# Optimization experiments

Hardware: AMD Instinct MI355X
Metric: run time of the kernel (lower is better)

## Reference

```python
import jax, jax.numpy as jnp
import numpy as np

N, K = 256, 133
INPUT_W, INPUT_H = 256, 256
SPLIT = 2.0
W = round(INPUT_W * SPLIT)  # 512
H = round(INPUT_H * SPLIT)  # 512
SIGMA = (5.66, 5.66)
BETA = 10.0
LABEL_BETA = 10.0


def setup_inputs() -> dict:
    key = jax.random.key(0)
    k1, k2, k3 = jax.random.split(key, 3)
    pred = jax.random.normal(k1, (N, K, W + H), dtype=jnp.float32)
    xy = jax.random.uniform(k2, (N, K, 2), dtype=jnp.float32) * INPUT_W
    vis = (jax.random.uniform(k3, (N, K, 1), dtype=jnp.float32) > 0.2).astype(jnp.float32)
    keypoints = jnp.concatenate([xy, vis], axis=-1)
    return {"pred": pred, "keypoints": keypoints}


def _gaussian_targets(keypoints):
    # Vectorized equivalent of the Python (n,k) loop in gaussian_smoothng.
    kp_xy = keypoints[..., :2]
    vis = keypoints[..., 2]
    mu = jnp.round(kp_xy * SPLIT)  # int64 in torch; rounded float is numerically identical
    rx = SIGMA[0] * 3.0
    ry = SIGMA[1] * 3.0
    left = mu[..., 0] - rx
    right = mu[..., 0] + rx + 1.0
    top = mu[..., 1] - ry
    bottom = mu[..., 1] + ry + 1.0
    oob = (left >= W) | (top >= H) | (right < 0) | (bottom < 0)
    visible = vis >= 0.5
    valid = visible & (~oob)
    x = jnp.arange(W, dtype=jnp.float32)
    y = jnp.arange(H, dtype=jnp.float32)
    gx = jnp.exp(-((x[None, None, :] - mu[..., 0:1]) ** 2) / (2.0 * SIGMA[0] ** 2))
    gy = jnp.exp(-((y[None, None, :] - mu[..., 1:2]) ** 2) / (2.0 * SIGMA[1] ** 2))
    target_x = jnp.where(valid[..., None], gx, 0.0)  # (N,K,W)
    target_y = jnp.where(valid[..., None], gy, 0.0)  # (N,K,H)
    # weight = visible value, zeroed if visible but out of bounds
    weight = jnp.where(visible & oob, 0.0, vis)
    return target_x, target_y, weight


def _criterion(p, t):
    # p, t: (N*K, L). KLDivLoss(reduction='none') then mean over dim=1.
    log_pt = jax.nn.log_softmax(p * BETA, axis=1)
    lab = jax.nn.softmax(t * LABEL_BETA, axis=1)  # strictly positive
    kl = lab * (jnp.log(lab) - log_pt)
    return kl.mean(axis=1)


def reference(pred, keypoints):
    n, k, _ = pred.shape
    split = pred.shape[-1] // 2
    pred_x = pred[..., :split].reshape(-1, split)
    pred_y = pred[..., split:].reshape(-1, pred.shape[-1] - split)
    gt_x, gt_y, w = _gaussian_targets(keypoints)
    w = w.reshape(-1)
    loss_x = (_criterion(pred_x, gt_x.reshape(-1, W)) * w).sum()
    loss_y = (_criterion(pred_y, gt_y.reshape(-1, H)) * w).sum()
    return (loss_x + loss_y) / k
```

## Files before the change

### kernel.cpp

```cpp
#include <hip/hip_runtime.h>
#include <math.h>

#define NKP 133
#define NROWS (256 * NKP)
#define RH_TOTAL (2 * NROWS)
#define NQUADS (RH_TOTAL / 4)
#define NBLOCKS 2048
#define NWAVES (NBLOCKS * 4)
#define C2P  14.4269504088896f
#define NK2  0.02251706f
#define RAD  16.98f
#define LN2f 0.69314718055994531f

static __device__ __forceinline__ float fexp2(float x) { return __builtin_amdgcn_exp2f(x); }
static __device__ __forceinline__ float frcp (float x) { return __builtin_amdgcn_rcpf(x); }

__global__ __launch_bounds__(256) void rtmcc_partial_kernel(
    const float* __restrict__ pred,
    const float* __restrict__ keypoints,
    float* __restrict__ partials)
{
    const int wave = threadIdx.x >> 6;
    const int lane = threadIdx.x & 63;
    const int g    = lane >> 4;
    const int l4   = lane & 15;
    const int h    = g & 1;
    __shared__ float t_em1[256];
    __shared__ float t_eg [256];
    __shared__ float lds[4];

    {
        const int t = threadIdx.x;
        const float d = (float)(t - 128);
        float em1 = 0.0f, eg = 0.0f;
        if (fabsf(d) <= 35.0f) {
            const float gg = fexp2(-d * d * NK2);
            const float e  = fexp2(gg * C2P);
            em1 = e - 1.0f; eg = e * gg;
        }
        t_em1[t] = em1; t_eg[t] = eg;
    }
    __syncthreads();

    float acc = 0.0f;
    const int wid = blockIdx.x * 4 + wave;

    int q = wid;
    {
        const int row = 2 * q + (g >> 1);
        float kx = keypoints[row * 3 + 0];
        float ky = keypoints[row * 3 + 1];
        float kv = keypoints[row * 3 + 2];

        for (; q < NQUADS; q += NWAVES) {
            const float kxc = kx, kyc = ky, kvc = kv;
            const int qn = q + NWAVES;
            if (qn < NQUADS) {
                const int rown = 2 * qn + (g >> 1);
                kx = keypoints[rown * 3 + 0];
                ky = keypoints[rown * 3 + 1];
                kv = keypoints[rown * 3 + 2];
            }

            const float mux = rintf(kxc * 2.0f);
            const float muy = rintf(kyc * 2.0f);
            const bool oob = (mux - RAD >= 512.0f) || (muy - RAD >= 512.0f) ||
                             (mux + RAD + 1.0f < 0.0f) || (muy + RAD + 1.0f < 0.0f);
            const bool visible = (kvc >= 0.5f);
            const float w = (visible && oob) ? 0.0f : kvc;
            const bool active = (w > 0.0f);

            float S = 0.0f, Zw = 0.0f, R = 0.0f;
            if (active) {
                const float* ph = pred + (size_t)(4 * q + g) * 512;

                float4 qv[8];
                #pragma unroll
                for (int v = 0; v < 8; ++v)
                    qv[v] = *reinterpret_cast<const float4*>(ph + v * 64 + l4 * 4);

                #pragma unroll
                for (int v = 0; v < 8; ++v) {
                    S += fexp2(C2P * qv[v].x) + fexp2(C2P * qv[v].y)
                       + fexp2(C2P * qv[v].z) + fexp2(C2P * qv[v].w);
                    R -= qv[v].x + qv[v].y + qv[v].z + qv[v].w;
                }

                const float mu = h ? muy : mux;
                const int mui = (int)mu;
                int ws = mui - 64; ws = ws < 0 ? 0 : (ws > 384 ? 384 : ws);
                #pragma unroll
                for (int v = 0; v < 8; ++v) {
                    const int idx = ws + l4 + v * 16;
                    const float pw = ph[idx];
                    int t = idx - mui + 128;
                    t = t < 0 ? 0 : (t > 255 ? 255 : t);
                    const float em1 = t_em1[t], eg = t_eg[t];
                    Zw += em1;
                    R  += eg - em1 * pw;
                }
            }

            #pragma unroll
            for (int off = 1; off < 16; off <<= 1) {
                S  += __shfl_xor(S,  off, 64);
                Zw += __shfl_xor(Zw, off, 64);
                R  += __shfl_xor(R,  off, 64);
            }

            if (active) {
                const float Z = 512.0f + Zw;
                acc += w * (10.0f * R * frcp(Z) + (__log2f(S) - __log2f(Z)) * LN2f);
            }
        }
    }

    acc *= (1.0f / (16.0f * 512.0f * 133.0f));
    #pragma unroll
    for (int off = 1; off < 64; off <<= 1) acc += __shfl_xor(acc, off, 64);
    if (lane == 0) lds[wave] = acc;
    __syncthreads();
    if (threadIdx.x == 0)
        partials[blockIdx.x] = lds[0] + lds[1] + lds[2] + lds[3];
}

__global__ __launch_bounds__(256) void rtmcc_reduce_kernel(
    const float* __restrict__ partials, float* __restrict__ out)
{
    __shared__ float lds[4];
    float s = 0.0f;
    for (int i = threadIdx.x; i < NBLOCKS; i += 256) s += partials[i];
    #pragma unroll
    for (int off = 1; off < 64; off <<= 1) s += __shfl_xor(s, off, 64);
    if ((threadIdx.x & 63) == 0) lds[threadIdx.x >> 6] = s;
    __syncthreads();
    if (threadIdx.x == 0) out[0] = lds[0] + lds[1] + lds[2] + lds[3];
}

extern "C" void kernel_launch(void* const* d_in, const int* in_sizes, int n_in,
                              void* d_out, int out_size, void* d_ws, size_t ws_size,
                              hipStream_t stream) {
    const float* pred = (const float*)d_in[0];
    const float* kpts = (const float*)d_in[1];
    float* out = (float*)d_out;
    float* partials = (float*)d_ws;

    rtmcc_partial_kernel<<<NBLOCKS, 256, 0, stream>>>(pred, kpts, partials);
    rtmcc_reduce_kernel<<<1, 256, 0, stream>>>(partials, out);
}
```

Before: 26.92 us.

## Unroll quad loop into explicit double-buffered loads with packed LDS table

Replaces the strided loop over quads with an explicit sequence of at most three iterations per wave. It issues the bulk float4 loads for the first two quads before computing either, so the memory latency of both overlaps. The two LDS lookup tables are packed into one float2 array so a single LDS read fetches both values. The exp-sum accumulation is split into two partial accumulators to shorten dependency chains. Holding two 8-float4 buffers raises register pressure. The code also hard-codes the assumption that each wave handles at most three quads, which the grid size satisfies.

```diff
diff --git a/kernel.cpp b/kernel.cpp
--- a/kernel.cpp
+++ b/kernel.cpp
@@ -24,9 +24,9 @@
     const int lane = threadIdx.x & 63;
     const int g    = lane >> 4;
     const int l4   = lane & 15;
+    const int gh   = g >> 1;
     const int h    = g & 1;
-    __shared__ float t_em1[256];
-    __shared__ float t_eg [256];
+    __shared__ float2 twb[256];
     __shared__ float lds[4];
 
     {
@@ -38,81 +38,97 @@
             const float e  = fexp2(gg * C2P);
             em1 = e - 1.0f; eg = e * gg;
         }
-        t_em1[t] = em1; t_eg[t] = eg;
+        twb[t] = make_float2(em1, eg);
     }
     __syncthreads();
 
+    const int wid = blockIdx.x * 4 + wave;
+    const int q0 = wid, q1 = wid + NWAVES, q2 = wid + 2 * NWAVES;
+    const bool has3 = (q2 < NQUADS);
+
+    const int r0 = 2 * q0 + gh, r1 = 2 * q1 + gh;
+    const float k0x = keypoints[r0*3+0], k0y = keypoints[r0*3+1], k0v = keypoints[r0*3+2];
+    const float k1x = keypoints[r1*3+0], k1y = keypoints[r1*3+1], k1v = keypoints[r1*3+2];
+    float k2x = 0.f, k2y = 0.f, k2v = 0.f;
+    if (has3) {
+        const int r2 = 2 * q2 + gh;
+        k2x = keypoints[r2*3+0]; k2y = keypoints[r2*3+1]; k2v = keypoints[r2*3+2];
+    }
+
     float acc = 0.0f;
-    const int wid = blockIdx.x * 4 + wave;
 
-    int q = wid;
-    {
-        const int row = 2 * q + (g >> 1);
-        float kx = keypoints[row * 3 + 0];
-        float ky = keypoints[row * 3 + 1];
-        float kv = keypoints[row * 3 + 2];
+    struct It { const float* ph; float w, mu; int mui, ws; bool act; };
+    auto decode = [&](float kx, float ky, float kv, int q) {
+        It it;
+        const float mux = rintf(kx * 2.0f);
+        const float muy = rintf(ky * 2.0f);
+        const bool oob = (mux - RAD >= 512.0f) || (muy - RAD >= 512.0f) ||
+                         (mux + RAD + 1.0f < 0.0f) || (muy + RAD + 1.0f < 0.0f);
+        const bool vis = (kv >= 0.5f);
+        it.w   = (vis && oob) ? 0.0f : kv;
+        it.act = (it.w > 0.0f);
+        it.mu  = h ? muy : mux;
+        it.mui = (int)it.mu;
+        int ws = it.mui - 64; it.ws = ws < 0 ? 0 : (ws > 384 ? 384 : ws);
+        it.ph  = pred + (size_t)(4 * q + g) * 512;
+        return it;
+    };
 
-        for (; q < NQUADS; q += NWAVES) {
-            const float kxc = kx, kyc = ky, kvc = kv;
-            const int qn = q + NWAVES;
-            if (qn < NQUADS) {
-                const int rown = 2 * qn + (g >> 1);
-                kx = keypoints[rown * 3 + 0];
-                ky = keypoints[rown * 3 + 1];
-                kv = keypoints[rown * 3 + 2];
-            }
+    auto loadbulk = [&](const It& it, float4 (&qv)[8]) {
+        if (it.act) {
+            #pragma unroll
+            for (int v = 0; v < 8; ++v)
+                qv[v] = *reinterpret_cast<const float4*>(it.ph + v * 64 + l4 * 4);
+        }
+    };
 
-            const float mux = rintf(kxc * 2.0f);
-            const float muy = rintf(kyc * 2.0f);
-            const bool oob = (mux - RAD >= 512.0f) || (muy - RAD >= 512.0f) ||
-                             (mux + RAD + 1.0f < 0.0f) || (muy + RAD + 1.0f < 0.0f);
-            const bool visible = (kvc >= 0.5f);
-            const float w = (visible && oob) ? 0.0f : kvc;
-            const bool active = (w > 0.0f);
-
-            float S = 0.0f, Zw = 0.0f, R = 0.0f;
-            if (active) {
-                const float* ph = pred + (size_t)(4 * q + g) * 512;
-
-                float4 qv[8];
-                #pragma unroll
-                for (int v = 0; v < 8; ++v)
-                    qv[v] = *reinterpret_cast<const float4*>(ph + v * 64 + l4 * 4);
-
-                #pragma unroll
-                for (int v = 0; v < 8; ++v) {
-                    S += fexp2(C2P * qv[v].x) + fexp2(C2P * qv[v].y)
-                       + fexp2(C2P * qv[v].z) + fexp2(C2P * qv[v].w);
-                    R -= qv[v].x + qv[v].y + qv[v].z + qv[v].w;
-                }
-
-                const float mu = h ? muy : mux;
-                const int mui = (int)mu;
-                int ws = mui - 64; ws = ws < 0 ? 0 : (ws > 384 ? 384 : ws);
-                #pragma unroll
-                for (int v = 0; v < 8; ++v) {
-                    const int idx = ws + l4 + v * 16;
-                    const float pw = ph[idx];
-                    int t = idx - mui + 128;
-                    t = t < 0 ? 0 : (t > 255 ? 255 : t);
-                    const float em1 = t_em1[t], eg = t_eg[t];
-                    Zw += em1;
-                    R  += eg - em1 * pw;
-                }
-            }
-
+    auto compute = [&](const It& it, const float4 (&qv)[8]) {
+        float s0 = 0.f, s1 = 0.f, r0 = 0.f, r1 = 0.f;
+        #pragma unroll
+        for (int v = 0; v < 8; v += 2) {
+            s0 += fexp2(C2P*qv[v].x) + fexp2(C2P*qv[v].y)
+                + fexp2(C2P*qv[v].z) + fexp2(C2P*qv[v].w);
+            r0 -= (qv[v].x + qv[v].y) + (qv[v].z + qv[v].w);
+            s1 += fexp2(C2P*qv[v+1].x) + fexp2(C2P*qv[v+1].y)
+                + fexp2(C2P*qv[v+1].z) + fexp2(C2P*qv[v+1].w);
+            r1 -= (qv[v+1].x + qv[v+1].y) + (qv[v+1].z + qv[v+1].w);
+        }
+        float S = s0 + s1, R = r0 + r1, Zw = 0.f;
+        if (it.act) {
             #pragma unroll
-            for (int off = 1; off < 16; off <<= 1) {
-                S  += __shfl_xor(S,  off, 64);
-                Zw += __shfl_xor(Zw, off, 64);
-                R  += __shfl_xor(R,  off, 64);
-            }
-
-            if (active) {
-                const float Z = 512.0f + Zw;
-                acc += w * (10.0f * R * frcp(Z) + (__log2f(S) - __log2f(Z)) * LN2f);
+            for (int v = 0; v < 8; ++v) {
+                const int idx = it.ws + l4 + v * 16;
+                const float pw = it.ph[idx];
+                int t = idx - it.mui + 128;
+                t = t < 0 ? 0 : (t > 255 ? 255 : t);
+                const float2 te = twb[t];
+                Zw += te.x;
+                R  += te.y - te.x * pw;
             }
         }
+        #pragma unroll
+        for (int off = 1; off < 16; off <<= 1) {
+            S  += __shfl_xor(S,  off, 64);
+            Zw += __shfl_xor(Zw, off, 64);
+            R  += __shfl_xor(R,  off, 64);
+        }
+        if (it.act) {
+            const float Z = 512.0f + Zw;
+            acc += it.w * (10.0f * R * frcp(Z) + (__log2f(S) - __log2f(Z)) * LN2f);
+        }
+    };
+
+    const It it0 = decode(k0x, k0y, k0v, q0);
+    const It it1 = decode(k1x, k1y, k1v, q1);
+    float4 A[8], B[8];
+    loadbulk(it0, A);
+    loadbulk(it1, B);
+    compute(it0, A);
+    compute(it1, B);
+    if (has3) {
+        const It it2 = decode(k2x, k2y, k2v, q2);
+        loadbulk(it2, A);
+        compute(it2, A);
     }
 
     acc *= (1.0f / (16.0f * 512.0f * 133.0f));
```

Result: slower. 28.89 us (+7.3%).

## Map one quad per wave across full grid, use DPP group sums and packed LUT

Applied to the files above, without the earlier changes.

Replaces the grid-stride loop over quads with a launch of NQUADS/4 blocks so each wave handles exactly one quad. The 16-lane shuffle reductions become DPP row-shift adds, with only lane 15 of each group holding the full sum. The two LDS lookup tables are packed into one float2 array, and the exp/sum accumulation is split into two chains. This removes loop overhead and shuffle latency, but the partials buffer and the single-block reduce grow from 2048 to about 4256 entries.

```diff
diff --git a/kernel.cpp b/kernel.cpp
--- a/kernel.cpp
+++ b/kernel.cpp
@@ -5,8 +5,7 @@
 #define NROWS (256 * NKP)
 #define RH_TOTAL (2 * NROWS)
 #define NQUADS (RH_TOTAL / 4)
-#define NBLOCKS 2048
-#define NWAVES (NBLOCKS * 4)
+#define NBLOCKS (NQUADS / 4)
 #define C2P  14.4269504088896f
 #define NK2  0.02251706f
 #define RAD  16.98f
@@ -14,6 +13,16 @@
 
 static __device__ __forceinline__ float fexp2(float x) { return __builtin_amdgcn_exp2f(x); }
 static __device__ __forceinline__ float frcp (float x) { return __builtin_amdgcn_rcpf(x); }
+
+#define DPP_SHR_ADD(x, CTRL)                                                   \
+    x += __int_as_float(__builtin_amdgcn_update_dpp(                           \
+            0, __float_as_int(x), (CTRL), 0xf, 0xf, true))
+#define GROUP_SUM(x) do {                                                      \
+    DPP_SHR_ADD(x, 0x111);                                      \
+    DPP_SHR_ADD(x, 0x112);                                      \
+    DPP_SHR_ADD(x, 0x114);                                      \
+    DPP_SHR_ADD(x, 0x118);                                      \
+} while (0)
 
 __global__ __launch_bounds__(256) void rtmcc_partial_kernel(
     const float* __restrict__ pred,
@@ -24,10 +33,16 @@
     const int lane = threadIdx.x & 63;
     const int g    = lane >> 4;
     const int l4   = lane & 15;
+    const int gh   = g >> 1;
     const int h    = g & 1;
-    __shared__ float t_em1[256];
-    __shared__ float t_eg [256];
+    __shared__ float2 twb[256];
     __shared__ float lds[4];
+
+    const int q   = blockIdx.x * 4 + wave;
+    const int row = 2 * q + gh;
+    const float kx = keypoints[row * 3 + 0];
+    const float ky = keypoints[row * 3 + 1];
+    const float kv = keypoints[row * 3 + 2];
 
     {
         const int t = threadIdx.x;
@@ -38,87 +53,68 @@
             const float e  = fexp2(gg * C2P);
             em1 = e - 1.0f; eg = e * gg;
         }
-        t_em1[t] = em1; t_eg[t] = eg;
+        twb[t] = make_float2(em1, eg);
     }
     __syncthreads();
 
-    float acc = 0.0f;
-    const int wid = blockIdx.x * 4 + wave;
+    const float mux = rintf(kx * 2.0f);
+    const float muy = rintf(ky * 2.0f);
+    const bool oob = (mux - RAD >= 512.0f) || (muy - RAD >= 512.0f) ||
+                     (mux + RAD + 1.0f < 0.0f) || (muy + RAD + 1.0f < 0.0f);
+    const bool visible = (kv >= 0.5f);
+    const float w = (visible && oob) ? 0.0f : kv;
+    const bool act = (w > 0.0f);
 
-    int q = wid;
-    {
-        const int row = 2 * q + (g >> 1);
-        float kx = keypoints[row * 3 + 0];
-        float ky = keypoints[row * 3 + 1];
-        float kv = keypoints[row * 3 + 2];
+    float S = 0.0f, Zw = 0.0f, R = 0.0f;
+    if (act) {
+        const float* ph = pred + (size_t)(4 * q + g) * 512;
 
-        for (; q < NQUADS; q += NWAVES) {
-            const float kxc = kx, kyc = ky, kvc = kv;
-            const int qn = q + NWAVES;
-            if (qn < NQUADS) {
-                const int rown = 2 * qn + (g >> 1);
-                kx = keypoints[rown * 3 + 0];
-                ky = keypoints[rown * 3 + 1];
-                kv = keypoints[rown * 3 + 2];
-            }
+        float4 qv[8];
+        #pragma unroll
+        for (int v = 0; v < 8; ++v)
+            qv[v] = *reinterpret_cast<const float4*>(ph + v * 64 + l4 * 4);
 
-            const float mux = rintf(kxc * 2.0f);
-            const float muy = rintf(kyc * 2.0f);
-            const bool oob = (mux - RAD >= 512.0f) || (muy - RAD >= 512.0f) ||
-                             (mux + RAD + 1.0f < 0.0f) || (muy + RAD + 1.0f < 0.0f);
-            const bool visible = (kvc >= 0.5f);
-            const float w = (visible && oob) ? 0.0f : kvc;
-            const bool active = (w > 0.0f);
+        float s0 = 0.f, s1 = 0.f, r0 = 0.f, r1 = 0.f;
+        #pragma unroll
+        for (int v = 0; v < 8; v += 2) {
+            s0 += fexp2(C2P*qv[v].x)   + fexp2(C2P*qv[v].y)
+                + fexp2(C2P*qv[v].z)   + fexp2(C2P*qv[v].w);
+            r0 -= (qv[v].x + qv[v].y) + (qv[v].z + qv[v].w);
+            s1 += fexp2(C2P*qv[v+1].x) + fexp2(C2P*qv[v+1].y)
+                + fexp2(C2P*qv[v+1].z) + fexp2(C2P*qv[v+1].w);
+            r1 -= (qv[v+1].x + qv[v+1].y) + (qv[v+1].z + qv[v+1].w);
+        }
+        S = s0 + s1; R = r0 + r1;
 
-            float S = 0.0f, Zw = 0.0f, R = 0.0f;
-            if (active) {
-                const float* ph = pred + (size_t)(4 * q + g) * 512;
-
-                float4 qv[8];
-                #pragma unroll
-                for (int v = 0; v < 8; ++v)
-                    qv[v] = *reinterpret_cast<const float4*>(ph + v * 64 + l4 * 4);
-
-                #pragma unroll
-                for (int v = 0; v < 8; ++v) {
-                    S += fexp2(C2P * qv[v].x) + fexp2(C2P * qv[v].y)
-                       + fexp2(C2P * qv[v].z) + fexp2(C2P * qv[v].w);
-                    R -= qv[v].x + qv[v].y + qv[v].z + qv[v].w;
-                }
-
-                const float mu = h ? muy : mux;
-                const int mui = (int)mu;
-                int ws = mui - 64; ws = ws < 0 ? 0 : (ws > 384 ? 384 : ws);
-                #pragma unroll
-                for (int v = 0; v < 8; ++v) {
-                    const int idx = ws + l4 + v * 16;
-                    const float pw = ph[idx];
-                    int t = idx - mui + 128;
-                    t = t < 0 ? 0 : (t > 255 ? 255 : t);
-                    const float em1 = t_em1[t], eg = t_eg[t];
-                    Zw += em1;
-                    R  += eg - em1 * pw;
-                }
-            }
-
-            #pragma unroll
-            for (int off = 1; off < 16; off <<= 1) {
-                S  += __shfl_xor(S,  off, 64);
-                Zw += __shfl_xor(Zw, off, 64);
-                R  += __shfl_xor(R,  off, 64);
-            }
-
-            if (active) {
-                const float Z = 512.0f + Zw;
-                acc += w * (10.0f * R * frcp(Z) + (__log2f(S) - __log2f(Z)) * LN2f);
-            }
+        const float mu = h ? muy : mux;
+        const int mui = (int)mu;
+        int ws = mui - 64; ws = ws < 0 ? 0 : (ws > 384 ? 384 : ws);
+        #pragma unroll
+        for (int v = 0; v < 8; ++v) {
+            const int idx = ws + l4 + v * 16;
+            const float pw = ph[idx];
+            int t = idx - mui + 128;
+            t = t < 0 ? 0 : (t > 255 ? 255 : t);
+            const float2 te = twb[t];
+            Zw += te.x;
+            R  += te.y - te.x * pw;
         }
     }
 
-    acc *= (1.0f / (16.0f * 512.0f * 133.0f));
+    GROUP_SUM(S);
+    GROUP_SUM(Zw);
+    GROUP_SUM(R);
+
+    float accv = 0.0f;
+    if (act && l4 == 15) {
+        const float Z = 512.0f + Zw;
+        accv = w * (10.0f * R * frcp(Z) + (__log2f(S) - __log2f(Z)) * LN2f)
+                 * (1.0f / (512.0f * 133.0f));
+    }
+
     #pragma unroll
-    for (int off = 1; off < 64; off <<= 1) acc += __shfl_xor(acc, off, 64);
-    if (lane == 0) lds[wave] = acc;
+    for (int off = 1; off < 64; off <<= 1) accv += __shfl_xor(accv, off, 64);
+    if (lane == 0) lds[wave] = accv;
     __syncthreads();
     if (threadIdx.x == 0)
         partials[blockIdx.x] = lds[0] + lds[1] + lds[2] + lds[3];
```

Measured after the change: 27.96 us. 1.04x slower.

## Fuse reduction via atomicAdd, shrink gaussian window to 80 taps, pack LUT

Applied to the files above, without the earlier changes.

Removes the second reduction kernel by having each block atomically add its partial sum into the output after a memset. The window correction loop shrinks from 128 to 80 taps with no index clamping, and the two lookup tables are packed into one float2 array. The exp accumulation is split into two chains, and the keypoint loads are hoisted above the table build. The changes target launch overhead and per-row work, at the cost of a memset launch, nondeterministic float atomics, and a narrower window that relies on the Gaussian being negligible beyond about 35 pixels.

```diff
diff --git a/kernel.cpp b/kernel.cpp
--- a/kernel.cpp
+++ b/kernel.cpp
@@ -11,23 +11,35 @@
 #define NK2  0.02251706f
 #define RAD  16.98f
 #define LN2f 0.69314718055994531f
+#define WTAPS 5
 
 static __device__ __forceinline__ float fexp2(float x) { return __builtin_amdgcn_exp2f(x); }
 static __device__ __forceinline__ float frcp (float x) { return __builtin_amdgcn_rcpf(x); }
 
-__global__ __launch_bounds__(256) void rtmcc_partial_kernel(
+__global__ __launch_bounds__(256) void rtmcc_kernel(
     const float* __restrict__ pred,
     const float* __restrict__ keypoints,
-    float* __restrict__ partials)
+    float* __restrict__ out)
 {
     const int wave = threadIdx.x >> 6;
     const int lane = threadIdx.x & 63;
     const int g    = lane >> 4;
     const int l4   = lane & 15;
+    const int gh   = g >> 1;
     const int h    = g & 1;
-    __shared__ float t_em1[256];
-    __shared__ float t_eg [256];
+    __shared__ float2 twb[256];
     __shared__ float lds[4];
+
+    float acc = 0.0f;
+    int q = blockIdx.x * 4 + wave;
+
+    float kx, ky, kv;
+    {
+        const int row = 2 * q + gh;
+        kx = keypoints[row * 3 + 0];
+        ky = keypoints[row * 3 + 1];
+        kv = keypoints[row * 3 + 2];
+    }
 
     {
         const int t = threadIdx.x;
@@ -38,80 +50,72 @@
             const float e  = fexp2(gg * C2P);
             em1 = e - 1.0f; eg = e * gg;
         }
-        t_em1[t] = em1; t_eg[t] = eg;
+        twb[t] = make_float2(em1, eg);
     }
     __syncthreads();
 
-    float acc = 0.0f;
-    const int wid = blockIdx.x * 4 + wave;
+    for (; q < NQUADS; q += NWAVES) {
+        const float kxc = kx, kyc = ky, kvc = kv;
+        const int qn = q + NWAVES;
+        if (qn < NQUADS) {
+            const int rown = 2 * qn + gh;
+            kx = keypoints[rown * 3 + 0];
+            ky = keypoints[rown * 3 + 1];
+            kv = keypoints[rown * 3 + 2];
+        }
 
-    int q = wid;
-    {
-        const int row = 2 * q + (g >> 1);
-        float kx = keypoints[row * 3 + 0];
-        float ky = keypoints[row * 3 + 1];
-        float kv = keypoints[row * 3 + 2];
+        const float mux = rintf(kxc * 2.0f);
+        const float muy = rintf(kyc * 2.0f);
+        const bool oob = (mux - RAD >= 512.0f) || (muy - RAD >= 512.0f) ||
+                         (mux + RAD + 1.0f < 0.0f) || (muy + RAD + 1.0f < 0.0f);
+        const bool visible = (kvc >= 0.5f);
+        const float w = (visible && oob) ? 0.0f : kvc;
+        const bool act = (w > 0.0f);
 
-        for (; q < NQUADS; q += NWAVES) {
-            const float kxc = kx, kyc = ky, kvc = kv;
-            const int qn = q + NWAVES;
-            if (qn < NQUADS) {
-                const int rown = 2 * qn + (g >> 1);
-                kx = keypoints[rown * 3 + 0];
-                ky = keypoints[rown * 3 + 1];
-                kv = keypoints[rown * 3 + 2];
+        float S = 0.0f, Zw = 0.0f, R = 0.0f;
+        if (act) {
+            const float* ph = pred + (size_t)(4 * q + g) * 512;
+
+            float4 qv[8];
+            #pragma unroll
+            for (int v = 0; v < 8; ++v)
+                qv[v] = *reinterpret_cast<const float4*>(ph + v * 64 + l4 * 4);
+
+            float s0 = 0.f, s1 = 0.f, r0 = 0.f, r1 = 0.f;
+            #pragma unroll
+            for (int v = 0; v < 8; v += 2) {
+                s0 += fexp2(C2P*qv[v].x)   + fexp2(C2P*qv[v].y)
+                    + fexp2(C2P*qv[v].z)   + fexp2(C2P*qv[v].w);
+                r0 -= (qv[v].x + qv[v].y) + (qv[v].z + qv[v].w);
+                s1 += fexp2(C2P*qv[v+1].x) + fexp2(C2P*qv[v+1].y)
+                    + fexp2(C2P*qv[v+1].z) + fexp2(C2P*qv[v+1].w);
+                r1 -= (qv[v+1].x + qv[v+1].y) + (qv[v+1].z + qv[v+1].w);
             }
+            S = s0 + s1; R = r0 + r1;
 
-            const float mux = rintf(kxc * 2.0f);
-            const float muy = rintf(kyc * 2.0f);
-            const bool oob = (mux - RAD >= 512.0f) || (muy - RAD >= 512.0f) ||
-                             (mux + RAD + 1.0f < 0.0f) || (muy + RAD + 1.0f < 0.0f);
-            const bool visible = (kvc >= 0.5f);
-            const float w = (visible && oob) ? 0.0f : kvc;
-            const bool active = (w > 0.0f);
+            const float mu = h ? muy : mux;
+            const int mui = (int)mu;
+            int ws = mui - 40; ws = ws < 0 ? 0 : (ws > 432 ? 432 : ws);
+            #pragma unroll
+            for (int v = 0; v < WTAPS; ++v) {
+                const int idx = ws + l4 + v * 16;
+                const float pw = ph[idx];
+                const float2 te = twb[idx - mui + 128];
+                Zw += te.x;
+                R  += te.y - te.x * pw;
+            }
+        }
 
-            float S = 0.0f, Zw = 0.0f, R = 0.0f;
-            if (active) {
-                const float* ph = pred + (size_t)(4 * q + g) * 512;
+        #pragma unroll
+        for (int off = 1; off < 16; off <<= 1) {
+            S  += __shfl_xor(S,  off, 64);
+            Zw += __shfl_xor(Zw, off, 64);
+            R  += __shfl_xor(R,  off, 64);
+        }
 
-                float4 qv[8];
-                #pragma unroll
-                for (int v = 0; v < 8; ++v)
-                    qv[v] = *reinterpret_cast<const float4*>(ph + v * 64 + l4 * 4);
-
-                #pragma unroll
-                for (int v = 0; v < 8; ++v) {
-                    S += fexp2(C2P * qv[v].x) + fexp2(C2P * qv[v].y)
-                       + fexp2(C2P * qv[v].z) + fexp2(C2P * qv[v].w);
-                    R -= qv[v].x + qv[v].y + qv[v].z + qv[v].w;
-                }
-
-                const float mu = h ? muy : mux;
-                const int mui = (int)mu;
-                int ws = mui - 64; ws = ws < 0 ? 0 : (ws > 384 ? 384 : ws);
-                #pragma unroll
-                for (int v = 0; v < 8; ++v) {
-                    const int idx = ws + l4 + v * 16;
-                    const float pw = ph[idx];
-                    int t = idx - mui + 128;
-                    t = t < 0 ? 0 : (t > 255 ? 255 : t);
-                    const float em1 = t_em1[t], eg = t_eg[t];
-                    Zw += em1;
-                    R  += eg - em1 * pw;
-                }
-            }
-
-            #pragma unroll
-            for (int off = 1; off < 16; off <<= 1) {
-                S  += __shfl_xor(S,  off, 64);
-                Zw += __shfl_xor(Zw, off, 64);
-                R  += __shfl_xor(R,  off, 64);
-            }
-
-            if (active) {
-                const float Z = 512.0f + Zw;
-                acc += w * (10.0f * R * frcp(Z) + (__log2f(S) - __log2f(Z)) * LN2f);
-            }
+        if (act) {
+            const float Z = 512.0f + Zw;
+            acc += w * (10.0f * R * frcp(Z) + (__log2f(S) - __log2f(Z)) * LN2f);
         }
     }
 
@@ -121,20 +125,7 @@
     if (lane == 0) lds[wave] = acc;
     __syncthreads();
     if (threadIdx.x == 0)
-        partials[blockIdx.x] = lds[0] + lds[1] + lds[2] + lds[3];
-}
-
-__global__ __launch_bounds__(256) void rtmcc_reduce_kernel(
-    const float* __restrict__ partials, float* __restrict__ out)
-{
-    __shared__ float lds[4];
-    float s = 0.0f;
-    for (int i = threadIdx.x; i < NBLOCKS; i += 256) s += partials[i];
-    #pragma unroll
-    for (int off = 1; off < 64; off <<= 1) s += __shfl_xor(s, off, 64);
-    if ((threadIdx.x & 63) == 0) lds[threadIdx.x >> 6] = s;
-    __syncthreads();
-    if (threadIdx.x == 0) out[0] = lds[0] + lds[1] + lds[2] + lds[3];
+        atomicAdd(out, lds[0] + lds[1] + lds[2] + lds[3]);
 }
 
 extern "C" void kernel_launch(void* const* d_in, const int* in_sizes, int n_in,
@@ -143,8 +134,7 @@
     const float* pred = (const float*)d_in[0];
     const float* kpts = (const float*)d_in[1];
     float* out = (float*)d_out;
-    float* partials = (float*)d_ws;
 
-    rtmcc_partial_kernel<<<NBLOCKS, 256, 0, stream>>>(pred, kpts, partials);
-    rtmcc_reduce_kernel<<<1, 256, 0, stream>>>(partials, out);
+    hipMemsetAsync(out, 0, sizeof(float), stream);
+    rtmcc_kernel<<<NBLOCKS, 256, 0, stream>>>(pred, kpts, out);
 }
```

Result: slower. 43.83 us (+62.8%).
